# Optimization experiments

Measured on AMD Instinct MI355X. Metric: run time of the kernel, lower is better.

Reference implementation:

```python
import jax, jax.numpy as jnp
import numpy as np

EPS = 1e-7
INF = 1e8
SOFT_CENTER_RADIUS = 3.0
TOPK = 13
IOU_WEIGHT = 3.0
NUM_CLASSES = 80
N_PRIORS = 33600
NUM_GT = 256
IMG = 1024.0


def setup_inputs() -> dict:
    key = jax.random.key(0)
    k1, k2, k3, k4, k5, k6, k7 = jax.random.split(key, 7)
    n, g, c = N_PRIORS, NUM_GT, NUM_CLASSES
    pred_scores = jax.random.normal(k1, (n, c), jnp.float32)
    # priors: (cx, cy, stride, stride)
    ctr = jax.random.uniform(k2, (n, 2), jnp.float32) * IMG
    stride = jnp.full((n, 1), 8.0, jnp.float32)
    priors = jnp.concatenate([ctr, stride, stride], axis=-1)
    # predicted boxes, x1y1x2y2
    pwh = jax.random.uniform(k3, (n, 2), jnp.float32) * 96.0 + 8.0
    pctr = jax.random.uniform(k4, (n, 2), jnp.float32) * IMG
    pred_bboxes = jnp.concatenate([pctr - pwh / 2, pctr + pwh / 2], axis=-1)
    # gt boxes, x1y1x2y2
    gwh = jax.random.uniform(k5, (g, 2), jnp.float32) * 192.0 + 16.0
    gctr = jax.random.uniform(k6, (g, 2), jnp.float32) * IMG
    gt_bboxes = jnp.concatenate([gctr - gwh / 2, gctr + gwh / 2], axis=-1)
    gt_labels = jax.random.randint(k7, (g,), 0, c, dtype=jnp.int32).astype(jnp.int64)
    return {"pred_scores": pred_scores, "priors": priors,
            "pred_bboxes": pred_bboxes, "gt_bboxes": gt_bboxes,
            "gt_labels": gt_labels}


def _pairwise_iou(a, b):
    # a: (n,4), b: (g,4), x1y1x2y2 -> (n,g)
    area_a = (a[:, 2] - a[:, 0]) * (a[:, 3] - a[:, 1])
    area_b = (b[:, 2] - b[:, 0]) * (b[:, 3] - b[:, 1])
    lt = jnp.maximum(a[:, None, :2], b[None, :, :2])
    rb = jnp.minimum(a[:, None, 2:], b[None, :, 2:])
    wh = jnp.clip(rb - lt, 0.0, None)
    inter = wh[..., 0] * wh[..., 1]
    union = area_a[:, None] + area_b[None, :] - inter
    return inter / jnp.maximum(union, 1e-6)


def reference(pred_scores, priors, pred_bboxes, gt_bboxes, gt_labels):
    n, g = pred_bboxes.shape[0], gt_bboxes.shape[0]
    gt_labels = gt_labels.astype(jnp.int32)

    # ---- find_inside_points (box_dim == 4) ----
    pts = priors[:, :2]                                   # (n,2)
    lt = pts[:, None, :] - gt_bboxes[None, :, :2]
    rb = gt_bboxes[None, :, 2:] - pts[:, None, :]
    is_in_gts = jnp.min(jnp.concatenate([lt, rb], -1), -1) > 0   # (n,g)
    pad_bbox_flag = gt_bboxes.sum(-1) > 0                        # (g,)
    is_in_gts = is_in_gts & pad_bbox_flag[None, :]
    valid_mask = jnp.any(is_in_gts, -1)                          # (n,)

    # ---- soft center prior ----
    gt_center = (gt_bboxes[:, :2] + gt_bboxes[:, 2:]) * 0.5      # (g,2)
    dist = jnp.sqrt(((pts[:, None, :] - gt_center[None, :, :]) ** 2).sum(-1))
    dist = dist / priors[:, 2:3]                                 # / stride
    dist = dist * valid_mask[:, None].astype(dist.dtype)
    soft_center_prior = jnp.power(10.0, dist - SOFT_CENTER_RADIUS)

    # ---- iou cost ----
    ious = _pairwise_iou(pred_bboxes, gt_bboxes)                 # (n,g)
    iou_cost = -jnp.log(ious + EPS) * IOU_WEIGHT

    # ---- soft classification cost (BCE-with-logits, iou targets) ----
    logits = pred_scores[:, gt_labels]                           # (n,g)
    scale = jnp.abs(ious - jax.nn.sigmoid(logits)) ** 2
    bce = jnp.maximum(logits, 0) - logits * ious + jnp.log1p(jnp.exp(-jnp.abs(logits)))
    cost = bce * scale + iou_cost + soft_center_prior
    cost = jnp.where(valid_mask[:, None], cost, INF)

    # ---- dynamic k matching (vectorized over GTs) ----
    K = min(TOPK, n)
    topk_ious, _ = jax.lax.top_k(ious.T, K)                      # (g,K)
    dynamic_ks = jnp.clip(topk_ious.sum(-1).astype(jnp.int32), 1, None)  # (g,)
    _, cand_idx = jax.lax.top_k(-cost.T, K)                      # (g,K) lowest-cost priors per gt
    sel = (jnp.arange(K)[None, :] < dynamic_ks[:, None]).astype(jnp.float32)
    matching = jnp.zeros((g, n), jnp.float32).at[
        jnp.arange(g)[:, None], cand_idx].set(sel).T             # (n,g)

    # resolve priors matched to multiple gts -> keep min-cost gt
    multi = matching.sum(-1) > 1
    onehot_min = jax.nn.one_hot(jnp.argmin(cost, -1), g, dtype=jnp.float32)
    matching = jnp.where(multi[:, None], onehot_min, matching)

    fg = matching.sum(-1) > 0
    matched_gt_inds = jnp.argmax(matching, -1)                   # (n,)
    matched_pred_ious = (matching * ious).sum(-1)                # (n,)

    final = fg & valid_mask
    assigned_gt_inds = jnp.where(final, matched_gt_inds + 1, 0)
    assigned_labels = jnp.where(final, gt_labels[matched_gt_inds], -1)
    max_overlaps = jnp.where(final, matched_pred_ious, -INF)
    return assigned_gt_inds, max_overlaps, assigned_labels
```

## Files before the change

kernel.cpp:

```cpp
#include <hip/hip_runtime.h>
#include <cstdint>

#define NPRI 33600
#define NGT  256
#define NCLS 80
#define KTOP 13
#define INF_F 1.0e8f
#define EPS_F 1e-7f
#define L10 3.3219280948873623f
#define SCN_T 1024
#define NW   (SCN_T / 64)
#define NIT  ((NPRI + SCN_T - 1) / SCN_T)
#define CAPI 4096
#define CAPC 1024
#define RFIX 5.5f
#define PREP_BLKS ((NPRI + 255) / 256)
#define NEGINF __int_as_float(0xff800000)

typedef unsigned long long u64;

__device__ __forceinline__ int get_label(const void* p, int j, int is64) {
    if (is64) return (int)((const long long*)p)[j];
    return ((const int*)p)[j];
}

__device__ __forceinline__ float wave_max_bc_f32(float v) {
    #pragma unroll
    for (int off = 32; off > 0; off >>= 1) v = fmaxf(v, __shfl_down(v, off, 64));
    return __int_as_float(__builtin_amdgcn_readfirstlane(__float_as_int(v)));
}
__device__ __forceinline__ u64 wave_min_bc_u64(u64 v) {
    #pragma unroll
    for (int off = 32; off > 0; off >>= 1) { u64 o = __shfl_down(v, off, 64); v = (o < v) ? o : v; }
    unsigned lo = (unsigned)__builtin_amdgcn_readfirstlane((int)(v & 0xffffffffull));
    unsigned hi = (unsigned)__builtin_amdgcn_readfirstlane((int)(v >> 32));
    return (((u64)hi) << 32) | lo;
}
template<int NSL>
__device__ __forceinline__ void wave_merge_max13_f32(float (&l)[NSL], float* dst, int lane) {
    int p = 0;
    for (int r = 0; r < KTOP; ++r) {
        float cur = NEGINF;
        #pragma unroll
        for (int s = 0; s < NSL; ++s) if (s == p) cur = l[NSL - 1 - s];
        float bm = wave_max_bc_f32(cur);
        u64 m = __ballot(cur == bm && bm != NEGINF);
        int first = __ffsll(m) - 1;
        if (lane == first) p++;
        if (lane == 0) dst[r] = bm;
    }
}
template<int NSL>
__device__ __forceinline__ void wave_merge_minN(u64 (&l)[NSL], u64* dst, int lane) {
    int p = 0;
    for (int r = 0; r < KTOP; ++r) {
        u64 cur = ~0ull;
        #pragma unroll
        for (int s = 0; s < NSL; ++s) if (s == p) cur = l[s];
        u64 bm = wave_min_bc_u64(cur);
        if (cur == bm && bm != ~0ull) p++;
        if (lane == 0) dst[r] = bm;
    }
}

__device__ __forceinline__ float iou_exact(float4 pb, float areap, float gx1, float gy1,
                                           float gx2, float gy2, float areag) {
    float iw = fmaxf(fminf(pb.z, gx2) - fmaxf(pb.x, gx1), 0.0f);
    float ih = fmaxf(fminf(pb.w, gy2) - fmaxf(pb.y, gy1), 0.0f);
    float inter = iw * ih;
    return inter / fmaxf(areap + areag - inter, 1e-6f);
}
__device__ __forceinline__ float cost_exact(float4 p2, float gcx, float gcy,
                                            float l, float iou) {
    float dx = p2.x - gcx, dy = p2.y - gcy;
    float dist = sqrtf(dx * dx + dy * dy) / p2.z;
    float soft = exp2f((dist - 3.0f) * L10);
    float sig = 1.0f / (1.0f + expf(-l));
    float dd = iou - sig;
    float bce = fmaxf(l, 0.0f) - l * iou + log1pf(expf(-fabsf(l)));
    float iouc = -logf(iou + EPS_F) * 3.0f;
    return bce * (dd * dd) + iouc + soft;
}

__global__ __launch_bounds__(256) void k_prep(
        const float* __restrict__ priors, const float* __restrict__ gt,
        const void* labels, const float* __restrict__ pboxes,
        float4* __restrict__ pbp,
        int* count, int* firstgt, int* flag) {
    __shared__ float4 gbox[NGT];
    __shared__ int    gpad[NGT];
    __shared__ int    bad;
    const int tid = threadIdx.x;
    const int b = blockIdx.x;
    if (b == 0 && tid == 0) bad = 0;
    {
        float4 bx = ((const float4*)gt)[tid];
        gbox[tid] = bx;
        gpad[tid] = ((bx.x + bx.y + bx.z + bx.w) > 0.0f) ? 1 : 0;
    }
    __syncthreads();
    if (b == 0 && tid < 128) {
        long long v = ((const long long*)labels)[tid];
        if (v < 0 || v >= NCLS) atomicOr(&bad, 1);
    }
    int i = b * 256 + tid;
    if (i < NPRI) {
        count[i] = 0; firstgt[i] = NGT;
        float4 pr = ((const float4*)priors)[i];
        float px = pr.x, py = pr.y;
        int v = 0;
        for (int j = 0; j < NGT; ++j) {
            float4 bx = gbox[j];
            float m = fminf(fminf(px - bx.x, py - bx.y), fminf(bx.z - px, bx.w - py));
            if (m > 0.0f && gpad[j]) { v = 1; break; }
        }
        pbp[2 * i]     = ((const float4*)pboxes)[i];
        pbp[2 * i + 1] = make_float4(px, py, pr.z, v ? 1.0f : 0.0f);
    }
    if (b == 0) {
        __syncthreads();
        if (tid == 0) *flag = bad ? 0 : 1;
    }
}

__global__ __launch_bounds__(SCN_T) void k_scan(
        const float* __restrict__ scores,
        const float4* __restrict__ pbp,
        const float* __restrict__ gt, const void* labels, const int* flag,
        int* count, int* firstgt) {
    const int tid = threadIdx.x, lane = tid & 63, wid = tid >> 6;
    const int j = blockIdx.x;
    const int is64 = *flag;

    const float4 gb = ((const float4*)gt)[j];
    const float gx1 = gb.x, gy1 = gb.y, gx2 = gb.z, gy2 = gb.w;
    const float areag = (gx2 - gx1) * (gy2 - gy1);
    const float gcx = (gx1 + gx2) * 0.5f, gcy = (gy1 + gy2) * 0.5f;
    const int lab = get_label(labels, j, is64);

    __shared__ int s_ni, s_nc, s_mode;
    __shared__ float s_dmax;
    __shared__ float liou[CAPI];
    __shared__ int lcost[CAPC];
    __shared__ float wiof[(NW - 1) * KTOP];
    __shared__ u64 wco[NW * KTOP];
    __shared__ u64 csel[KTOP];
    __shared__ float s_iou13[KTOP];
    if (tid == 0) { s_ni = 0; s_nc = 0; }
    __syncthreads();

    {
        const int i0 = tid;
        const int ia1 = i0 + SCN_T;
        float4 pb_c = pbp[2 * i0],  p2_c = pbp[2 * i0 + 1];
        float4 pb_n = pbp[2 * ia1], p2_n = pbp[2 * ia1 + 1];
        for (int it = 0; it < NIT; ++it) {
            int i = i0 + it * SCN_T;
            int ipre = i + 2 * SCN_T;
            int ic = (ipre < NPRI) ? ipre : i0;
            float4 pb_p = pbp[2 * ic];
            float4 p2_p = pbp[2 * ic + 1];

            bool inb = (i < NPRI);
            float iou = 0.0f;
            bool pc = false;
            if (inb) {
                float areap = (pb_c.z - pb_c.x) * (pb_c.w - pb_c.y);
                float iw = fmaxf(fminf(pb_c.z, gx2) - fmaxf(pb_c.x, gx1), 0.0f);
                float ih = fmaxf(fminf(pb_c.w, gy2) - fmaxf(pb_c.y, gy1), 0.0f);
                float inter = iw * ih;
                iou = inter / fmaxf(areap + areag - inter, 1e-6f);
                if (p2_c.w != 0.0f) {
                    float dx = p2_c.x - gcx, dy = p2_c.y - gcy;
                    float rad = p2_c.z * RFIX;
                    pc = (dx * dx + dy * dy <= rad * rad * (1.0f + 1e-5f));
                }
            }
            if (inb && iou > 0.0f) {
                int p = atomicAdd(&s_ni, 1);
                if (p < CAPI) liou[p] = iou;
            }
            if (pc) {
                int p = atomicAdd(&s_nc, 1);
                if (p < CAPC) lcost[p] = i;
            }
            pb_c = pb_n; p2_c = p2_n;
            pb_n = pb_p; p2_n = p2_p;
        }
    }
    __syncthreads();
    const int ni = s_ni, nc = s_nc;
    const int ncc = (nc < CAPC) ? nc : CAPC;
    const bool fI = (ni > CAPI);

    if (wid == 0) {
        u64 lf[KTOP];
        #pragma unroll
        for (int s = 0; s < KTOP; ++s) lf[s] = ~0ull;
        for (int k = lane; k < ncc; k += 64) {
            int i = lcost[k];
            float4 pb = pbp[2 * i];
            float4 p2 = pbp[2 * i + 1];
            float areap = (pb.z - pb.x) * (pb.w - pb.y);
            float iou = iou_exact(pb, areap, gx1, gy1, gx2, gy2, areag);
            float ec = cost_exact(p2, gcx, gcy, scores[(size_t)i * NCLS + lab], iou);
            u64 ck = (((u64)__float_as_uint(ec)) << 32) | (unsigned)i;
            if (ck < lf[KTOP - 1]) {
                lf[KTOP - 1] = ck;
                #pragma unroll
                for (int s = KTOP - 1; s > 0; --s)
                    if (lf[s] < lf[s - 1]) { u64 t = lf[s]; lf[s] = lf[s - 1]; lf[s - 1] = t; }
            }
        }
        wave_merge_minN<KTOP>(lf, csel, lane);
        if (lane == 0) {
            u64 tk = csel[KTOP - 1];
            int mode; float dmax = 0.0f;
            if (tk == ~0ull) mode = 2;
            else {
                float tau = __uint_as_float((unsigned)(tk >> 32));
                if (!(tau < 9.0e7f)) mode = 2;
                else {
                    dmax = 3.0f + __log2f(tau + 1e-5f) * (1.0f / L10) + 4e-3f;
                    mode = (dmax > RFIX || nc > CAPC) ? 1 : 0;
                }
            }
            s_mode = mode; s_dmax = dmax;
        }
    } else if (!fI) {
        float lf[KTOP];
        #pragma unroll
        for (int s = 0; s < KTOP; ++s) lf[s] = NEGINF;
        for (int k = (wid - 1) * 64 + lane; k < ni; k += 64 * (NW - 1)) {
            float v = liou[k];
            if (v > lf[0]) {
                lf[0] = v;
                #pragma unroll
                for (int s = 0; s < KTOP - 1; ++s)
                    if (lf[s] > lf[s + 1]) { float t = lf[s]; lf[s] = lf[s + 1]; lf[s + 1] = t; }
            }
        }
        wave_merge_max13_f32<KTOP>(lf, &wiof[(wid - 1) * KTOP], lane);
    }
    __syncthreads();

    if (fI) {
        if (wid > 0) {
            float lf[KTOP];
            #pragma unroll
            for (int s = 0; s < KTOP; ++s) lf[s] = NEGINF;
            for (int i = (wid - 1) * 64 + lane; i < NPRI; i += 64 * (NW - 1)) {
                float4 pb = pbp[2 * i];
                float areap = (pb.z - pb.x) * (pb.w - pb.y);
                float iou = iou_exact(pb, areap, gx1, gy1, gx2, gy2, areag);
                if (iou > 0.0f && iou > lf[0]) {
                    lf[0] = iou;
                    #pragma unroll
                    for (int s = 0; s < KTOP - 1; ++s)
                        if (lf[s] > lf[s + 1]) { float t = lf[s]; lf[s] = lf[s + 1]; lf[s + 1] = t; }
                }
            }
            wave_merge_max13_f32<KTOP>(lf, &wiof[(wid - 1) * KTOP], lane);
        }
        __syncthreads();
    }

    if (wid == 0) {
        int p = 0;
        for (int r = 0; r < KTOP; ++r) {
            float cur = (lane < NW - 1 && p < KTOP) ? wiof[lane * KTOP + p] : NEGINF;
            float bm = wave_max_bc_f32(cur);
            u64 m = __ballot(cur == bm && bm != NEGINF);
            int first = __ffsll(m) - 1;
            if (lane == first) p++;
            if (lane == 0) s_iou13[r] = bm;
        }
    }

    int mode = s_mode;
    if (mode == 1) {
        const float dmax = s_dmax;
        if (tid == 0) s_nc = 0;
        __syncthreads();
        for (int i = tid; i < NPRI; i += SCN_T) {
            float4 p2 = pbp[2 * i + 1];
            if (p2.w != 0.0f) {
                float dx = p2.x - gcx, dy = p2.y - gcy;
                float rad = p2.z * dmax;
                if (dx * dx + dy * dy <= rad * rad * (1.0f + 1e-5f)) {
                    int p = atomicAdd(&s_nc, 1);
                    if (p < CAPC) lcost[p] = i;
                }
            }
        }
        __syncthreads();
        int nc2 = s_nc;
        if (nc2 <= CAPC) {
            if (wid == 0) {
                u64 lf[KTOP];
                #pragma unroll
                for (int s = 0; s < KTOP; ++s) lf[s] = ~0ull;
                for (int k = lane; k < nc2; k += 64) {
                    int i = lcost[k];
                    float4 pb = pbp[2 * i];
                    float4 p2 = pbp[2 * i + 1];
                    float areap = (pb.z - pb.x) * (pb.w - pb.y);
                    float iou = iou_exact(pb, areap, gx1, gy1, gx2, gy2, areag);
                    float ec = cost_exact(p2, gcx, gcy, scores[(size_t)i * NCLS + lab], iou);
                    u64 ck = (((u64)__float_as_uint(ec)) << 32) | (unsigned)i;
                    if (ck < lf[KTOP - 1]) {
                        lf[KTOP - 1] = ck;
                        #pragma unroll
                        for (int s = KTOP - 1; s > 0; --s)
                            if (lf[s] < lf[s - 1]) { u64 t = lf[s]; lf[s] = lf[s - 1]; lf[s - 1] = t; }
                    }
                }
                wave_merge_minN<KTOP>(lf, csel, lane);
            }
        } else {
            mode = 2;
        }
        __syncthreads();
    }
    if (mode == 2) {
        u64 lf[KTOP];
        #pragma unroll
        for (int s = 0; s < KTOP; ++s) lf[s] = ~0ull;
        for (int i = tid; i < NPRI; i += SCN_T) {
            float4 pb = pbp[2 * i];
            float4 p2 = pbp[2 * i + 1];
            float areap = (pb.z - pb.x) * (pb.w - pb.y);
            float iou = iou_exact(pb, areap, gx1, gy1, gx2, gy2, areag);
            float ec = INF_F;
            if (p2.w != 0.0f) ec = cost_exact(p2, gcx, gcy, scores[(size_t)i * NCLS + lab], iou);
            u64 k2 = (((u64)__float_as_uint(ec)) << 32) | (unsigned)i;
            if (k2 < lf[KTOP - 1]) {
                lf[KTOP - 1] = k2;
                #pragma unroll
                for (int s = KTOP - 1; s > 0; --s)
                    if (lf[s] < lf[s - 1]) { u64 t = lf[s]; lf[s] = lf[s - 1]; lf[s - 1] = t; }
            }
        }
        wave_merge_minN<KTOP>(lf, &wco[wid * KTOP], lane);
        __syncthreads();
        if (wid == 0) {
            int p = 0;
            for (int r = 0; r < KTOP; ++r) {
                u64 cur = (lane < NW && p < KTOP) ? wco[lane * KTOP + p] : ~0ull;
                u64 bm = wave_min_bc_u64(cur);
                if (cur == bm && bm != ~0ull) p++;
                if (lane == 0) csel[r] = bm;
            }
        }
        __syncthreads();
    }

    __syncthreads();
    if (wid == 0) {
        float tsum = 0.0f;
        #pragma unroll
        for (int r = 0; r < KTOP; ++r) {
            float v = s_iou13[r];
            tsum += (v == NEGINF) ? 0.0f : v;
        }
        int ks = (int)tsum;
        if (ks < 1) ks = 1;
        if (lane < KTOP && lane < ks) {
            u64 mine = csel[lane];
            if (mine != ~0ull) {
                int idx = (int)(unsigned)(mine & 0xFFFFFFFFull);
                atomicAdd(&count[idx], 1);
                atomicMin(&firstgt[idx], j);
            }
        }
    }
}

__global__ __launch_bounds__(256) void k_assign(
        const float* __restrict__ scores,
        const float4* __restrict__ pbp, const float* __restrict__ gt,
        const void* labels, const int* flag,
        const int* __restrict__ count, const int* __restrict__ firstgt,
        float* __restrict__ out) {
    __shared__ float4 gbox[NGT];
    __shared__ int glab[NGT];
    __shared__ float gcxs[NGT], gcys[NGT], gareas[NGT];
    __shared__ int s_nm;
    __shared__ int s_mlist[256];
    __shared__ u64 red4[4];
    const int tid = threadIdx.x;
    const int is64 = *flag;
    {
        float4 b = ((const float4*)gt)[tid];
        gbox[tid] = b;
        glab[tid] = get_label(labels, tid, is64);
        gcxs[tid] = (b.x + b.z) * 0.5f;
        gcys[tid] = (b.y + b.w) * 0.5f;
        gareas[tid] = (b.z - b.x) * (b.w - b.y);
    }
    if (tid == 0) s_nm = 0;
    __syncthreads();
    const int i = blockIdx.x * 256 + tid;
    const bool act = (i < NPRI);
    if (act) {
        float4 p2 = pbp[2 * i + 1];
        int v = (p2.w != 0.0f) ? 1 : 0;
        int c = count[i];
        float o0 = 0.0f, o1 = -INF_F, o2 = -1.0f;
        if (v && c == 1) {
            int j = firstgt[i];
            float4 pb = pbp[2 * i];
            float areap = (pb.z - pb.x) * (pb.w - pb.y);
            float4 g = gbox[j];
            float iw = fmaxf(fminf(pb.z, g.z) - fmaxf(pb.x, g.x), 0.0f);
            float ih = fmaxf(fminf(pb.w, g.w) - fmaxf(pb.y, g.y), 0.0f);
            float inter = iw * ih;
            float iou = inter / fmaxf(areap + gareas[j] - inter, 1e-6f);
            o0 = (float)(j + 1); o1 = iou; o2 = (float)glab[j];
        } else if (v && c > 1) {
            int p = atomicAdd(&s_nm, 1);
            s_mlist[p] = i;
        }
        out[i] = o0;
        out[NPRI + i] = o1;
        out[2 * NPRI + i] = o2;
    }
    __syncthreads();
    const int nm = s_nm;
    const int j = tid;
    for (int m = 0; m < nm; ++m) {
        const int ii = s_mlist[m];
        float4 pb = pbp[2 * ii];
        float4 p2 = pbp[2 * ii + 1];
        float areap = (pb.z - pb.x) * (pb.w - pb.y);

        float4 g = gbox[j];
        float iw = fmaxf(fminf(pb.z, g.z) - fmaxf(pb.x, g.x), 0.0f);
        float ih = fmaxf(fminf(pb.w, g.w) - fmaxf(pb.y, g.y), 0.0f);
        float inter = iw * ih;
        float iou = inter / fmaxf(areap + gareas[j] - inter, 1e-6f);
        float dx = p2.x - gcxs[j], dy = p2.y - gcys[j];
        float dist = sqrtf(dx * dx + dy * dy) / p2.z;
        float soft = exp2f((dist - 3.0f) * L10);
        float l = scores[(size_t)ii * NCLS + glab[j]];
        float sig = 1.0f / (1.0f + expf(-l));
        float dd = iou - sig;
        float bce = fmaxf(l, 0.0f) - l * iou + log1pf(expf(-fabsf(l)));
        float cost = bce * (dd * dd) + (-logf(iou + EPS_F) * 3.0f) + soft;

        u64 key = (((u64)__float_as_uint(cost)) << 32) | (unsigned)j;
        u64 v = key;
        #pragma unroll
        for (int off = 32; off > 0; off >>= 1) {
            u64 o = __shfl_down(v, off, 64);
            v = (o < v) ? o : v;
        }
        if ((tid & 63) == 0) red4[tid >> 6] = v;
        __syncthreads();
        u64 best = red4[0];
        #pragma unroll
        for (int q = 1; q < 4; ++q) best = (red4[q] < best) ? red4[q] : best;
        if (key == best) {
            out[ii] = (float)(j + 1);
            out[NPRI + ii] = iou;
            out[2 * NPRI + ii] = (float)glab[j];
        }
        __syncthreads();
    }
}

extern "C" void kernel_launch(void* const* d_in, const int* in_sizes, int n_in,
                              void* d_out, int out_size, void* d_ws, size_t ws_size,
                              hipStream_t stream) {
    const float* scores = (const float*)d_in[0];
    const float* priors = (const float*)d_in[1];
    const float* pboxes = (const float*)d_in[2];
    const float* gt     = (const float*)d_in[3];
    const void*  labels = d_in[4];
    float* out = (float*)d_out;

    char* ws = (char*)d_ws;
    size_t off = 0;
    auto alloc = [&](size_t bytes) { size_t o = off; off = (off + bytes + 255) & ~(size_t)255; return o; };
    int*    flag     = (int*)(ws + alloc(4));
    int*    count    = (int*)(ws + alloc((size_t)NPRI * 4));
    int*    firstgt  = (int*)(ws + alloc((size_t)NPRI * 4));
    float4* pbp      = (float4*)(ws + alloc((size_t)NPRI * 32));
    (void)ws_size;

    hipLaunchKernelGGL(k_prep, dim3(PREP_BLKS), dim3(256), 0, stream,
                       priors, gt, labels, pboxes, pbp, count, firstgt, flag);
    hipLaunchKernelGGL(k_scan, dim3(NGT), dim3(SCN_T), 0, stream,
                       scores, pbp, gt, labels, flag, count, firstgt);
    hipLaunchKernelGGL(k_assign, dim3((NPRI + 255) / 256), dim3(256), 0, stream,
                       scores, pbp, gt, labels, flag, count, firstgt, out);
}
```

Baseline: 140.1 us.

## Keep per-thread IoU top-13 in registers during scan and deepen prefetch

The scan loop now keeps a running top-13 IoU list in registers per thread instead of appending positive IoUs to a shared-memory buffer with atomics and re-scanning it afterwards. This removes the shared-atomic append, the second selection pass and the overflow fallback path. The loop is also unrolled four ways with a four-deep register prefetch of prior data. The cost is extra register pressure from the 13-entry list plus four pairs of float4 buffers, and the final merge is now moved to wave 1 so it runs alongside wave 0's cost selection.

```diff
diff --git a/kernel.cpp b/kernel.cpp
--- a/kernel.cpp
+++ b/kernel.cpp
@@ -10,8 +10,6 @@
 #define L10 3.3219280948873623f
 #define SCN_T 1024
 #define NW   (SCN_T / 64)
-#define NIT  ((NPRI + SCN_T - 1) / SCN_T)
-#define CAPI 4096
 #define CAPC 1024
 #define RFIX 5.5f
 #define PREP_BLKS ((NPRI + 255) / 256)
@@ -35,6 +33,12 @@
     unsigned lo = (unsigned)__builtin_amdgcn_readfirstlane((int)(v & 0xffffffffull));
     unsigned hi = (unsigned)__builtin_amdgcn_readfirstlane((int)(v >> 32));
     return (((u64)hi) << 32) | lo;
+}
+__device__ __forceinline__ void insert_max13(float (&l)[KTOP], float v) {
+    l[0] = v;
+    #pragma unroll
+    for (int s = 0; s < KTOP - 1; ++s)
+        if (l[s] > l[s + 1]) { float t = l[s]; l[s] = l[s + 1]; l[s + 1] = t; }
 }
 template<int NSL>
 __device__ __forceinline__ void wave_merge_max13_f32(float (&l)[NSL], float* dst, int lane) {
@@ -123,6 +127,31 @@
     }
 }
 
+#define STEP(K, PB, P2) { \
+    const int i = i0 + (it + K) * SCN_T; \
+    float4 pbc = PB; float4 p2c = P2; \
+    int ip = i + 4 * SCN_T; \
+    int ic = (ip < NPRI) ? ip : i0; \
+    PB = pbp[2 * ic]; \
+    P2 = pbp[2 * ic + 1]; \
+    if (i < NPRI) { \
+        float areap = (pbc.z - pbc.x) * (pbc.w - pbc.y); \
+        float iw = fmaxf(fminf(pbc.z, gx2) - fmaxf(pbc.x, gx1), 0.0f); \
+        float ih = fmaxf(fminf(pbc.w, gy2) - fmaxf(pbc.y, gy1), 0.0f); \
+        float inter = iw * ih; \
+        float iou = inter / fmaxf(areap + areag - inter, 1e-6f); \
+        if (iou > 0.0f && iou > lfi[0]) insert_max13(lfi, iou); \
+        if (p2c.w != 0.0f) { \
+            float dx = p2c.x - gcx, dy = p2c.y - gcy; \
+            float rad = p2c.z * RFIX; \
+            if (dx * dx + dy * dy <= rad * rad * (1.0f + 1e-5f)) { \
+                int p = atomicAdd(&s_nc, 1); \
+                if (p < CAPC) lcost[p] = i; \
+            } \
+        } \
+    } \
+}
+
 __global__ __launch_bounds__(SCN_T) void k_scan(
         const float* __restrict__ scores,
         const float4* __restrict__ pbp,
@@ -138,60 +167,38 @@
     const float gcx = (gx1 + gx2) * 0.5f, gcy = (gy1 + gy2) * 0.5f;
     const int lab = get_label(labels, j, is64);
 
-    __shared__ int s_ni, s_nc, s_mode;
+    __shared__ int s_nc, s_mode;
     __shared__ float s_dmax;
-    __shared__ float liou[CAPI];
     __shared__ int lcost[CAPC];
-    __shared__ float wiof[(NW - 1) * KTOP];
+    __shared__ float wiof[NW * KTOP];
     __shared__ u64 wco[NW * KTOP];
     __shared__ u64 csel[KTOP];
     __shared__ float s_iou13[KTOP];
-    if (tid == 0) { s_ni = 0; s_nc = 0; }
-    __syncthreads();
-
+    if (tid == 0) s_nc = 0;
+    __syncthreads();
+
+    float lfi[KTOP];
+    #pragma unroll
+    for (int s = 0; s < KTOP; ++s) lfi[s] = NEGINF;
     {
         const int i0 = tid;
-        const int ia1 = i0 + SCN_T;
-        float4 pb_c = pbp[2 * i0],  p2_c = pbp[2 * i0 + 1];
-        float4 pb_n = pbp[2 * ia1], p2_n = pbp[2 * ia1 + 1];
-        for (int it = 0; it < NIT; ++it) {
-            int i = i0 + it * SCN_T;
-            int ipre = i + 2 * SCN_T;
-            int ic = (ipre < NPRI) ? ipre : i0;
-            float4 pb_p = pbp[2 * ic];
-            float4 p2_p = pbp[2 * ic + 1];
-
-            bool inb = (i < NPRI);
-            float iou = 0.0f;
-            bool pc = false;
-            if (inb) {
-                float areap = (pb_c.z - pb_c.x) * (pb_c.w - pb_c.y);
-                float iw = fmaxf(fminf(pb_c.z, gx2) - fmaxf(pb_c.x, gx1), 0.0f);
-                float ih = fmaxf(fminf(pb_c.w, gy2) - fmaxf(pb_c.y, gy1), 0.0f);
-                float inter = iw * ih;
-                iou = inter / fmaxf(areap + areag - inter, 1e-6f);
-                if (p2_c.w != 0.0f) {
-                    float dx = p2_c.x - gcx, dy = p2_c.y - gcy;
-                    float rad = p2_c.z * RFIX;
-                    pc = (dx * dx + dy * dy <= rad * rad * (1.0f + 1e-5f));
-                }
-            }
-            if (inb && iou > 0.0f) {
-                int p = atomicAdd(&s_ni, 1);
-                if (p < CAPI) liou[p] = iou;
-            }
-            if (pc) {
-                int p = atomicAdd(&s_nc, 1);
-                if (p < CAPC) lcost[p] = i;
-            }
-            pb_c = pb_n; p2_c = p2_n;
-            pb_n = pb_p; p2_n = p2_p;
-        }
-    }
-    __syncthreads();
-    const int ni = s_ni, nc = s_nc;
+        float4 pb0 = pbp[2 * i0],               p20 = pbp[2 * i0 + 1];
+        float4 pb1 = pbp[2 * (i0 + SCN_T)],     p21 = pbp[2 * (i0 + SCN_T) + 1];
+        float4 pb2 = pbp[2 * (i0 + 2 * SCN_T)], p22 = pbp[2 * (i0 + 2 * SCN_T) + 1];
+        float4 pb3 = pbp[2 * (i0 + 3 * SCN_T)], p23 = pbp[2 * (i0 + 3 * SCN_T) + 1];
+        for (int it = 0; it < 36; it += 4) {
+            STEP(0, pb0, p20)
+            STEP(1, pb1, p21)
+            STEP(2, pb2, p22)
+            STEP(3, pb3, p23)
+        }
+    }
+    __syncthreads();
+    const int nc = s_nc;
     const int ncc = (nc < CAPC) ? nc : CAPC;
-    const bool fI = (ni > CAPI);
+
+    wave_merge_max13_f32<KTOP>(lfi, &wiof[wid * KTOP], lane);
+    __syncthreads();
 
     if (wid == 0) {
         u64 lf[KTOP];
@@ -227,48 +234,10 @@
             }
             s_mode = mode; s_dmax = dmax;
         }
-    } else if (!fI) {
-        float lf[KTOP];
-        #pragma unroll
-        for (int s = 0; s < KTOP; ++s) lf[s] = NEGINF;
-        for (int k = (wid - 1) * 64 + lane; k < ni; k += 64 * (NW - 1)) {
-            float v = liou[k];
-            if (v > lf[0]) {
-                lf[0] = v;
-                #pragma unroll
-                for (int s = 0; s < KTOP - 1; ++s)
-                    if (lf[s] > lf[s + 1]) { float t = lf[s]; lf[s] = lf[s + 1]; lf[s + 1] = t; }
-            }
-        }
-        wave_merge_max13_f32<KTOP>(lf, &wiof[(wid - 1) * KTOP], lane);
-    }
-    __syncthreads();
-
-    if (fI) {
-        if (wid > 0) {
-            float lf[KTOP];
-            #pragma unroll
-            for (int s = 0; s < KTOP; ++s) lf[s] = NEGINF;
-            for (int i = (wid - 1) * 64 + lane; i < NPRI; i += 64 * (NW - 1)) {
-                float4 pb = pbp[2 * i];
-                float areap = (pb.z - pb.x) * (pb.w - pb.y);
-                float iou = iou_exact(pb, areap, gx1, gy1, gx2, gy2, areag);
-                if (iou > 0.0f && iou > lf[0]) {
-                    lf[0] = iou;
-                    #pragma unroll
-                    for (int s = 0; s < KTOP - 1; ++s)
-                        if (lf[s] > lf[s + 1]) { float t = lf[s]; lf[s] = lf[s + 1]; lf[s + 1] = t; }
-                }
-            }
-            wave_merge_max13_f32<KTOP>(lf, &wiof[(wid - 1) * KTOP], lane);
-        }
-        __syncthreads();
-    }
-
-    if (wid == 0) {
+    } else if (wid == 1) {
         int p = 0;
         for (int r = 0; r < KTOP; ++r) {
-            float cur = (lane < NW - 1 && p < KTOP) ? wiof[lane * KTOP + p] : NEGINF;
+            float cur = (lane < NW && p < KTOP) ? wiof[lane * KTOP + p] : NEGINF;
             float bm = wave_max_bc_f32(cur);
             u64 m = __ballot(cur == bm && bm != NEGINF);
             int first = __ffsll(m) - 1;
@@ -276,6 +245,7 @@
             if (lane == 0) s_iou13[r] = bm;
         }
     }
+    __syncthreads();
 
     int mode = s_mode;
     if (mode == 1) {
@@ -355,7 +325,6 @@
         __syncthreads();
     }
 
-    __syncthreads();
     if (wid == 0) {
         float tsum = 0.0f;
         #pragma unroll
```

Measured after the change: 149.2 us. 6.5% more time.

## Pad prior buffer, unroll scan loop 4x with deeper prefetch, precompute radius threshold

Applied to the files above, without the earlier changes.

The prior buffer gets a padded tail of dummy entries, so the main scan loop in k_scan can drop its per-iteration bounds checks. The loop is unrolled four ways with four in-flight prefetched loads instead of two, and only a single bounds-checked tail iteration remains. The prep kernel now stores the squared centre radius threshold (or -1 for invalid priors) in the validity slot, which removes a multiply and a branch per pair. The risks are a larger workspace and the sign-based validity test that every consumer must now use consistently.

```diff
diff --git a/kernel.cpp b/kernel.cpp
--- a/kernel.cpp
+++ b/kernel.cpp
@@ -10,10 +10,10 @@
 #define L10 3.3219280948873623f
 #define SCN_T 1024
 #define NW   (SCN_T / 64)
-#define NIT  ((NPRI + SCN_T - 1) / SCN_T)
 #define CAPI 4096
 #define CAPC 1024
 #define RFIX 5.5f
+#define NPAD (4 * SCN_T)
 #define PREP_BLKS ((NPRI + 255) / 256)
 #define NEGINF __int_as_float(0xff800000)
 
@@ -103,10 +103,14 @@
         long long v = ((const long long*)labels)[tid];
         if (v < 0 || v >= NCLS) atomicOr(&bad, 1);
     }
-    int i = b * 256 + tid;
-    if (i < NPRI) {
-        count[i] = 0; firstgt[i] = NGT;
-        float4 pr = ((const float4*)priors)[i];
+    int g = b * 256 + tid;
+    if (g < NPAD) {
+        pbp[2 * (NPRI + g)]     = make_float4(0.f, 0.f, 0.f, 0.f);
+        pbp[2 * (NPRI + g) + 1] = make_float4(0.f, 0.f, 1.f, -1.0f);
+    }
+    if (g < NPRI) {
+        count[g] = 0; firstgt[g] = NGT;
+        float4 pr = ((const float4*)priors)[g];
         float px = pr.x, py = pr.y;
         int v = 0;
         for (int j = 0; j < NGT; ++j) {
@@ -114,13 +118,37 @@
             float m = fminf(fminf(px - bx.x, py - bx.y), fminf(bx.z - px, bx.w - py));
             if (m > 0.0f && gpad[j]) { v = 1; break; }
         }
-        pbp[2 * i]     = ((const float4*)pboxes)[i];
-        pbp[2 * i + 1] = make_float4(px, py, pr.z, v ? 1.0f : 0.0f);
+        float rad = pr.z * RFIX;
+        float w = v ? rad * rad * (1.0f + 1e-5f) : -1.0f;
+        pbp[2 * g]     = ((const float4*)pboxes)[g];
+        pbp[2 * g + 1] = make_float4(px, py, pr.z, w);
     }
     if (b == 0) {
         __syncthreads();
         if (tid == 0) *flag = bad ? 0 : 1;
     }
+}
+
+#define STEPM(K, PB, P2) { \
+    const int i = i0 + (it + K) * SCN_T; \
+    float4 pbc = PB; float4 p2c = P2; \
+    const int ip = i + 4 * SCN_T; \
+    PB = pbp[2 * ip]; \
+    P2 = pbp[2 * ip + 1]; \
+    float areap = (pbc.z - pbc.x) * (pbc.w - pbc.y); \
+    float iw = fmaxf(fminf(pbc.z, gx2) - fmaxf(pbc.x, gx1), 0.0f); \
+    float ih = fmaxf(fminf(pbc.w, gy2) - fmaxf(pbc.y, gy1), 0.0f); \
+    float inter = iw * ih; \
+    float iou = inter / fmaxf(areap + areag - inter, 1e-6f); \
+    if (iou > 0.0f) { \
+        int p = atomicAdd(&s_ni, 1); \
+        if (p < CAPI) liou[p] = iou; \
+    } \
+    float dx = p2c.x - gcx, dy = p2c.y - gcy; \
+    if (dx * dx + dy * dy <= p2c.w) { \
+        int p = atomicAdd(&s_nc, 1); \
+        if (p < CAPC) lcost[p] = i; \
+    } \
 }
 
 __global__ __launch_bounds__(SCN_T) void k_scan(
@@ -151,41 +179,35 @@
 
     {
         const int i0 = tid;
-        const int ia1 = i0 + SCN_T;
-        float4 pb_c = pbp[2 * i0],  p2_c = pbp[2 * i0 + 1];
-        float4 pb_n = pbp[2 * ia1], p2_n = pbp[2 * ia1 + 1];
-        for (int it = 0; it < NIT; ++it) {
-            int i = i0 + it * SCN_T;
-            int ipre = i + 2 * SCN_T;
-            int ic = (ipre < NPRI) ? ipre : i0;
-            float4 pb_p = pbp[2 * ic];
-            float4 p2_p = pbp[2 * ic + 1];
-
-            bool inb = (i < NPRI);
-            float iou = 0.0f;
-            bool pc = false;
-            if (inb) {
-                float areap = (pb_c.z - pb_c.x) * (pb_c.w - pb_c.y);
-                float iw = fmaxf(fminf(pb_c.z, gx2) - fmaxf(pb_c.x, gx1), 0.0f);
-                float ih = fmaxf(fminf(pb_c.w, gy2) - fmaxf(pb_c.y, gy1), 0.0f);
+        float4 pb0 = pbp[2 * i0],               p20 = pbp[2 * i0 + 1];
+        float4 pb1 = pbp[2 * (i0 + SCN_T)],     p21 = pbp[2 * (i0 + SCN_T) + 1];
+        float4 pb2 = pbp[2 * (i0 + 2 * SCN_T)], p22 = pbp[2 * (i0 + 2 * SCN_T) + 1];
+        float4 pb3 = pbp[2 * (i0 + 3 * SCN_T)], p23 = pbp[2 * (i0 + 3 * SCN_T) + 1];
+        for (int it = 0; it < 32; it += 4) {
+            STEPM(0, pb0, p20)
+            STEPM(1, pb1, p21)
+            STEPM(2, pb2, p22)
+            STEPM(3, pb3, p23)
+        }
+        {
+            const int i = i0 + 32 * SCN_T;
+            if (i < NPRI) {
+                float4 pbc = pb0; float4 p2c = p20;
+                float areap = (pbc.z - pbc.x) * (pbc.w - pbc.y);
+                float iw = fmaxf(fminf(pbc.z, gx2) - fmaxf(pbc.x, gx1), 0.0f);
+                float ih = fmaxf(fminf(pbc.w, gy2) - fmaxf(pbc.y, gy1), 0.0f);
                 float inter = iw * ih;
-                iou = inter / fmaxf(areap + areag - inter, 1e-6f);
-                if (p2_c.w != 0.0f) {
-                    float dx = p2_c.x - gcx, dy = p2_c.y - gcy;
-                    float rad = p2_c.z * RFIX;
-                    pc = (dx * dx + dy * dy <= rad * rad * (1.0f + 1e-5f));
+                float iou = inter / fmaxf(areap + areag - inter, 1e-6f);
+                if (iou > 0.0f) {
+                    int p = atomicAdd(&s_ni, 1);
+                    if (p < CAPI) liou[p] = iou;
                 }
-            }
-            if (inb && iou > 0.0f) {
-                int p = atomicAdd(&s_ni, 1);
-                if (p < CAPI) liou[p] = iou;
-            }
-            if (pc) {
-                int p = atomicAdd(&s_nc, 1);
-                if (p < CAPC) lcost[p] = i;
-            }
-            pb_c = pb_n; p2_c = p2_n;
-            pb_n = pb_p; p2_n = p2_p;
+                float dx = p2c.x - gcx, dy = p2c.y - gcy;
+                if (dx * dx + dy * dy <= p2c.w) {
+                    int p = atomicAdd(&s_nc, 1);
+                    if (p < CAPC) lcost[p] = i;
+                }
+            }
         }
     }
     __syncthreads();
@@ -231,7 +253,8 @@
         float lf[KTOP];
         #pragma unroll
         for (int s = 0; s < KTOP; ++s) lf[s] = NEGINF;
-        for (int k = (wid - 1) * 64 + lane; k < ni; k += 64 * (NW - 1)) {
+        int nn = (ni < CAPI) ? ni : CAPI;
+        for (int k = (wid - 1) * 64 + lane; k < nn; k += 64 * (NW - 1)) {
             float v = liou[k];
             if (v > lf[0]) {
                 lf[0] = v;
@@ -284,7 +307,7 @@
         __syncthreads();
         for (int i = tid; i < NPRI; i += SCN_T) {
             float4 p2 = pbp[2 * i + 1];
-            if (p2.w != 0.0f) {
+            if (p2.w > 0.0f) {
                 float dx = p2.x - gcx, dy = p2.y - gcy;
                 float rad = p2.z * dmax;
                 if (dx * dx + dy * dy <= rad * rad * (1.0f + 1e-5f)) {
@@ -332,7 +355,7 @@
             float areap = (pb.z - pb.x) * (pb.w - pb.y);
             float iou = iou_exact(pb, areap, gx1, gy1, gx2, gy2, areag);
             float ec = INF_F;
-            if (p2.w != 0.0f) ec = cost_exact(p2, gcx, gcy, scores[(size_t)i * NCLS + lab], iou);
+            if (p2.w > 0.0f) ec = cost_exact(p2, gcx, gcy, scores[(size_t)i * NCLS + lab], iou);
             u64 k2 = (((u64)__float_as_uint(ec)) << 32) | (unsigned)i;
             if (k2 < lf[KTOP - 1]) {
                 lf[KTOP - 1] = k2;
@@ -404,7 +427,7 @@
     const bool act = (i < NPRI);
     if (act) {
         float4 p2 = pbp[2 * i + 1];
-        int v = (p2.w != 0.0f) ? 1 : 0;
+        int v = (p2.w > 0.0f) ? 1 : 0;
         int c = count[i];
         float o0 = 0.0f, o1 = -INF_F, o2 = -1.0f;
         if (v && c == 1) {
@@ -485,7 +508,7 @@
     int*    flag     = (int*)(ws + alloc(4));
     int*    count    = (int*)(ws + alloc((size_t)NPRI * 4));
     int*    firstgt  = (int*)(ws + alloc((size_t)NPRI * 4));
-    float4* pbp      = (float4*)(ws + alloc((size_t)NPRI * 32));
+    float4* pbp      = (float4*)(ws + alloc((size_t)(NPRI + NPAD) * 32));
     (void)ws_size;
 
     hipLaunchKernelGGL(k_prep, dim3(PREP_BLKS), dim3(256), 0, stream,
```

New measurement: 145.1 us. 3.6% more time.
